# Optimization experiments

Hardware: AMD Instinct MI355X
Metric: run time of the kernel (lower is better)

## Reference

```python
import jax, jax.numpy as jnp
import numpy as np


def setup_inputs() -> dict:
    key = jax.random.key(0)
    ks = jax.random.split(key, 8)
    shapes = [(128, 1, 334, 200), (128, 1, 167, 100), (128, 1, 84, 50),
              (128, 1, 42, 25), (128, 1, 21, 13)]
    # sparsity masks (post-sigmoid / gumbel activations), values in [0,1)
    hs = {f"h{i}": jax.random.uniform(ks[i], s, dtype=jnp.float32)
          for i, s in enumerate(shapes)}
    B, M = 128, 64
    im_dimx, im_dimy = 800, 1333
    # xyxy boxes in image coords: top-left in [0, 0.8*dim), size in [8, 0.2*dim+8)
    x1 = jax.random.uniform(ks[5], (B, M), dtype=jnp.float32) * (0.8 * im_dimx)
    y1 = jax.random.uniform(ks[6], (B, M), dtype=jnp.float32) * (0.8 * im_dimy)
    wh = jax.random.uniform(ks[7], (B, M, 2), dtype=jnp.float32)
    x2 = jnp.minimum(x1 + 8.0 + wh[..., 0] * (0.2 * im_dimx), im_dimx)
    y2 = jnp.minimum(y1 + 8.0 + wh[..., 1] * (0.2 * im_dimy), im_dimy)
    boxes = jnp.stack([x1, y1, x2, y2], axis=-1)  # [B, M, 4]
    inp = dict(hs)
    inp["boxes"] = boxes
    inp["im_dimx"] = im_dimx
    inp["im_dimy"] = im_dimy
    return inp


def _level_loss(hi, boxes, im_dimx, im_dimy):
    # hi: [B, 1, H, W], boxes: [B, M, 4] xyxy in image coords
    B, _, H, W = hi.shape
    scale_x = W / im_dimx
    scale_y = H / im_dimy
    x1 = jnp.clip(jnp.round(boxes[..., 0] * scale_x), 0, W - 1)  # [B, M]
    y1 = jnp.clip(jnp.round(boxes[..., 1] * scale_y), 0, H - 1)
    x2 = jnp.clip(jnp.round(boxes[..., 2] * scale_x), 0, W)
    y2 = jnp.clip(jnp.round(boxes[..., 3] * scale_y), 0, H)
    valid = (x2 > x1) & (y2 > y1)  # degenerate boxes skipped
    ys = jnp.arange(H, dtype=hi.dtype)[None, None, :]
    xs = jnp.arange(W, dtype=hi.dtype)[None, None, :]
    # separable per-box interval indicators; OR over boxes via count > 0
    row = ((ys >= y1[..., None]) & (ys < y2[..., None]) & valid[..., None]).astype(hi.dtype)  # [B,M,H]
    col = ((xs >= x1[..., None]) & (xs < x2[..., None])).astype(hi.dtype)                    # [B,M,W]
    cover = jnp.einsum('bmh,bmw->bhw', row, col)  # overlap count per pixel
    gt = (cover > 0).astype(hi.dtype)             # rectangle fill with 1
    tn_pixel = B * H * W
    pi = jnp.sum(gt) / tn_pixel
    return (jnp.sum(hi) / tn_pixel - pi) ** 2


def reference(h0, h1, h2, h3, h4, boxes, im_dimx, im_dimy):
    hs = (h0, h1, h2, h3, h4)
    losses = [_level_loss(hi, boxes, im_dimx, im_dimy) for hi in hs]
    return sum(losses) / len(losses)
```

## Files before the change

kernel.cpp:

```cpp
#include <hip/hip_runtime.h>

#define NLEV 5
#define BATCH 128
#define NBOX 64

__device__ __constant__ int c_H[NLEV] = {334, 167, 84, 42, 21};
__device__ __constant__ int c_N4[NLEV] = {2137600, 534400, 134400, 33600, 8736};
__device__ __constant__ int c_sb_base[NLEV + 1] = {0, 512, 640, 672, 688, 696};
__device__ __constant__ int c_cb_base[NLEV + 1] = {0, 128, 256, 299, 321, 332};

#define NSUMB 696
#define NCOVB 332
#define NBLOCKS (NSUMB + NCOVB)

#define COV_OFF_BYTES (NSUMB * 8)

__device__ inline unsigned long long maskn(int n) {
  return (n >= 64) ? ~0ull : ((1ull << n) - 1ull);
}
__device__ inline unsigned long long rangemask(int x1, int x2, int base) {
  int lo = min(max(x1 - base, 0), 64);
  int hi = min(max(x2 - base, 0), 64);
  return maskn(hi) & ~maskn(lo);
}

template <int H, int W, int BPB>
__device__ __forceinline__ int cover_compute(
    int lblk, const float* __restrict__ boxes, int dimx, int dimy, int t,
    unsigned long long* __restrict__ s_mask, int2* __restrict__ s_y) {
  constexpr int NW = (W + 63) / 64;
  const float sx = (float)((double)W / (double)dimx);
  const float sy = (float)((double)H / (double)dimy);
  const int b0 = lblk * BPB;

  for (int idx = t; idx < NBOX * BPB; idx += 256) {
    const int m = idx / BPB;
    const int j = idx - m * BPB;
    const int b = b0 + j;
    unsigned long long w[NW];
#pragma unroll
    for (int q = 0; q < NW; ++q) w[q] = 0ull;
    int y1 = 0, y2 = 0;
    if (b < BATCH) {
      const float* bp = boxes + ((size_t)b * NBOX + m) * 4;
      float fx1 = rintf(bp[0] * sx);
      float fy1 = rintf(bp[1] * sy);
      float fx2 = rintf(bp[2] * sx);
      float fy2 = rintf(bp[3] * sy);
      int x1 = (int)fminf(fmaxf(fx1, 0.0f), (float)(W - 1));
      int x2 = (int)fminf(fmaxf(fx2, 0.0f), (float)W);
      y1 = (int)fminf(fmaxf(fy1, 0.0f), (float)(H - 1));
      y2 = (int)fminf(fmaxf(fy2, 0.0f), (float)H);
      if ((x2 > x1) && (y2 > y1)) {
#pragma unroll
        for (int q = 0; q < NW; ++q) w[q] = rangemask(x1, x2, q * 64);
      } else {
        y1 = 0; y2 = 0;
      }
    }
#pragma unroll
    for (int q = 0; q < NW; ++q) s_mask[idx * NW + q] = w[q];
    s_y[idx] = make_int2(y1, y2);
  }
  __syncthreads();

  int local = 0;
  if (BPB == 1) {
    for (int h = t; h < H; h += 256) {
      unsigned long long acc[NW];
#pragma unroll
      for (int q = 0; q < NW; ++q) acc[q] = 0ull;
      for (int m = 0; m < NBOX; ++m) {
        const int2 yr = s_y[m];
        const unsigned long long ym =
            (h >= yr.x && h < yr.y) ? ~0ull : 0ull;
#pragma unroll
        for (int q = 0; q < NW; ++q) acc[q] |= s_mask[m * NW + q] & ym;
      }
#pragma unroll
      for (int q = 0; q < NW; ++q) local += __popcll(acc[q]);
    }
  } else {
    const int j = t / H;
    const int h = t - j * H;
    if (j < BPB && b0 + j < BATCH) {
      unsigned long long acc = 0ull;
      for (int m = 0; m < NBOX; ++m) {
        const int2 yr = s_y[m * BPB + j];
        const unsigned long long ym =
            (h >= yr.x && h < yr.y) ? ~0ull : 0ull;
        acc |= s_mask[m * BPB + j] & ym;
      }
      local = __popcll(acc);
    }
  }
  return local;
}

__global__ __launch_bounds__(256) void fused_kernel(
    const float* __restrict__ h0, const float* __restrict__ h1,
    const float* __restrict__ h2, const float* __restrict__ h3,
    const float* __restrict__ h4, const float* __restrict__ boxes,
    const int* __restrict__ dimx, const int* __restrict__ dimy,
    void* __restrict__ ws) {
  __shared__ unsigned long long s_mask[NBOX * 12];
  __shared__ int2 s_y[NBOX * 12];
  __shared__ double s_red[4];
  __shared__ int s_cnt[4];

  double* __restrict__ sum_part = (double*)ws;
  unsigned int* __restrict__ cov_part =
      (unsigned int*)((char*)ws + COV_OFF_BYTES);
  const int blk = blockIdx.x;
  const int t = threadIdx.x;

  if (blk < NSUMB) {
    int lev = 0;
    while (blk >= c_sb_base[lev + 1]) ++lev;
    const int lblk = blk - c_sb_base[lev];
    const int nblk = c_sb_base[lev + 1] - c_sb_base[lev];
    const float* p;
    switch (lev) {
      case 0: p = h0; break;
      case 1: p = h1; break;
      case 2: p = h2; break;
      case 3: p = h3; break;
      default: p = h4; break;
    }
    const float4* __restrict__ p4 = (const float4*)p;
    const int n4 = c_N4[lev];
    const int stride = nblk * 256;

    double acc = 0.0;
    for (int i = lblk * 256 + t; i < n4; i += stride) {
      float4 v = p4[i];
      acc += (double)v.x;
      acc += (double)v.y;
      acc += (double)v.z;
      acc += (double)v.w;
    }
    for (int off = 32; off > 0; off >>= 1) acc += __shfl_down(acc, off, 64);
    const int wave = t >> 6, lane = t & 63;
    if (lane == 0) s_red[wave] = acc;
    __syncthreads();
    if (t == 0)
      sum_part[blk] = (s_red[0] + s_red[1]) + (s_red[2] + s_red[3]);
  } else {
    const int cb = blk - NSUMB;
    const int dx = dimx[0], dy = dimy[0];
    int local;
    if (cb < c_cb_base[1]) {
      local = cover_compute<334, 200, 1>(cb, boxes, dx, dy, t, s_mask, s_y);
    } else if (cb < c_cb_base[2]) {
      local = cover_compute<167, 100, 1>(cb - 128, boxes, dx, dy, t, s_mask, s_y);
    } else if (cb < c_cb_base[3]) {
      local = cover_compute<84, 50, 3>(cb - 256, boxes, dx, dy, t, s_mask, s_y);
    } else if (cb < c_cb_base[4]) {
      local = cover_compute<42, 25, 6>(cb - 299, boxes, dx, dy, t, s_mask, s_y);
    } else {
      local = cover_compute<21, 13, 12>(cb - 321, boxes, dx, dy, t, s_mask, s_y);
    }
    for (int off = 32; off > 0; off >>= 1) local += __shfl_down(local, off, 64);
    const int wave = t >> 6, lane = t & 63;
    if (lane == 0) s_cnt[wave] = local;
    __syncthreads();
    if (t == 0)
      cov_part[cb] =
          (unsigned int)(s_cnt[0] + s_cnt[1] + s_cnt[2] + s_cnt[3]);
  }
}

__global__ __launch_bounds__(320) void final_kernel(
    const void* __restrict__ ws, float* __restrict__ out) {
  const double* __restrict__ sum_part = (const double*)ws;
  const unsigned int* __restrict__ cov_part =
      (const unsigned int*)((const char*)ws + COV_OFF_BYTES);
  const int wave = threadIdx.x >> 6;
  const int lane = threadIdx.x & 63;
  __shared__ double s_loss[NLEV];
  __device__ __constant__ static const int dummy = 0; (void)dummy;

  const int sb0 = c_sb_base[wave], sb1 = c_sb_base[wave + 1];
  double s = 0.0;
  for (int i = sb0 + lane; i < sb1; i += 64) s += sum_part[i];
  const int cb0 = c_cb_base[wave], cb1 = c_cb_base[wave + 1];
  unsigned int c = 0;
  for (int i = cb0 + lane; i < cb1; i += 64) c += cov_part[i];
  for (int off = 32; off > 0; off >>= 1) {
    s += __shfl_down(s, off, 64);
    c += __shfl_down(c, off, 64);
  }
  if (lane == 0) {
    const int HH[NLEV] = {334, 167, 84, 42, 21};
    const int WW[NLEV] = {200, 100, 50, 25, 13};
    double tn = (double)BATCH * (double)HH[wave] * (double)WW[wave];
    double d = s / tn - (double)c / tn;
    s_loss[wave] = d * d;
  }
  __syncthreads();
  if (threadIdx.x == 0) {
    double acc = 0.0;
    for (int l = 0; l < NLEV; ++l) acc += s_loss[l];
    out[0] = (float)(acc / (double)NLEV);
  }
}

extern "C" void kernel_launch(void* const* d_in, const int* in_sizes, int n_in,
                              void* d_out, int out_size, void* d_ws,
                              size_t ws_size, hipStream_t stream) {
  const float* h0 = (const float*)d_in[0];
  const float* h1 = (const float*)d_in[1];
  const float* h2 = (const float*)d_in[2];
  const float* h3 = (const float*)d_in[3];
  const float* h4 = (const float*)d_in[4];
  const float* boxes = (const float*)d_in[5];
  const int* dimx = (const int*)d_in[6];
  const int* dimy = (const int*)d_in[7];

  fused_kernel<<<NBLOCKS, 256, 0, stream>>>(h0, h1, h2, h3, h4, boxes, dimx,
                                            dimy, d_ws);
  final_kernel<<<1, 320, 0, stream>>>(d_ws, (float*)d_out);
}
```

Baseline: 96.07 us.

## Fuse final reduction into main kernel via cooperative grid sync

Launches the main kernel cooperatively and uses a grid-wide sync so block 0 can perform the final per-level loss reduction, removing the separate second kernel launch. The sum block count is trimmed so the grid can be co-resident (1024 blocks). A fallback keeps the two-kernel path if the cooperative launch fails. The grid sync adds barrier cost and the cooperative launch may carry extra launch overhead.

```diff
diff --git a/kernel.cpp b/kernel.cpp
--- a/kernel.cpp
+++ b/kernel.cpp
@@ -1,15 +1,19 @@
 #include <hip/hip_runtime.h>
+#include <hip/hip_cooperative_groups.h>
+
+namespace cg = cooperative_groups;
 
 #define NLEV 5
 #define BATCH 128
 #define NBOX 64
 
 __device__ __constant__ int c_H[NLEV] = {334, 167, 84, 42, 21};
+__device__ __constant__ int c_W[NLEV] = {200, 100, 50, 25, 13};
 __device__ __constant__ int c_N4[NLEV] = {2137600, 534400, 134400, 33600, 8736};
-__device__ __constant__ int c_sb_base[NLEV + 1] = {0, 512, 640, 672, 688, 696};
+__device__ __constant__ int c_sb_base[NLEV + 1] = {0, 508, 636, 668, 684, 692};
 __device__ __constant__ int c_cb_base[NLEV + 1] = {0, 128, 256, 299, 321, 332};
 
-#define NSUMB 696
+#define NSUMB 692
 #define NCOVB 332
 #define NBLOCKS (NSUMB + NCOVB)
 
@@ -22,6 +26,19 @@
   int lo = min(max(x1 - base, 0), 64);
   int hi = min(max(x2 - base, 0), 64);
   return maskn(hi) & ~maskn(lo);
+}
+
+__device__ inline void store_agent(double* p, double v) {
+  __hip_atomic_store(p, v, __ATOMIC_RELAXED, __HIP_MEMORY_SCOPE_AGENT);
+}
+__device__ inline void store_agent(unsigned int* p, unsigned int v) {
+  __hip_atomic_store(p, v, __ATOMIC_RELAXED, __HIP_MEMORY_SCOPE_AGENT);
+}
+__device__ inline double load_agent(const double* p) {
+  return __hip_atomic_load(p, __ATOMIC_RELAXED, __HIP_MEMORY_SCOPE_AGENT);
+}
+__device__ inline unsigned int load_agent(const unsigned int* p) {
+  return __hip_atomic_load(p, __ATOMIC_RELAXED, __HIP_MEMORY_SCOPE_AGENT);
 }
 
 template <int H, int W, int BPB>
@@ -72,8 +89,7 @@
       for (int q = 0; q < NW; ++q) acc[q] = 0ull;
       for (int m = 0; m < NBOX; ++m) {
         const int2 yr = s_y[m];
-        const unsigned long long ym =
-            (h >= yr.x && h < yr.y) ? ~0ull : 0ull;
+        const unsigned long long ym = (h >= yr.x && h < yr.y) ? ~0ull : 0ull;
 #pragma unroll
         for (int q = 0; q < NW; ++q) acc[q] |= s_mask[m * NW + q] & ym;
       }
@@ -87,8 +103,7 @@
       unsigned long long acc = 0ull;
       for (int m = 0; m < NBOX; ++m) {
         const int2 yr = s_y[m * BPB + j];
-        const unsigned long long ym =
-            (h >= yr.x && h < yr.y) ? ~0ull : 0ull;
+        const unsigned long long ym = (h >= yr.x && h < yr.y) ? ~0ull : 0ull;
         acc |= s_mask[m * BPB + j] & ym;
       }
       local = __popcll(acc);
@@ -97,22 +112,25 @@
   return local;
 }
 
-__global__ __launch_bounds__(256) void fused_kernel(
+template <bool COOP>
+__global__ __launch_bounds__(256) void fused_t(
     const float* __restrict__ h0, const float* __restrict__ h1,
     const float* __restrict__ h2, const float* __restrict__ h3,
     const float* __restrict__ h4, const float* __restrict__ boxes,
     const int* __restrict__ dimx, const int* __restrict__ dimy,
-    void* __restrict__ ws) {
+    void* __restrict__ ws, float* __restrict__ out) {
   __shared__ unsigned long long s_mask[NBOX * 12];
   __shared__ int2 s_y[NBOX * 12];
   __shared__ double s_red[4];
   __shared__ int s_cnt[4];
+  __shared__ double s_loss[NLEV];
 
   double* __restrict__ sum_part = (double*)ws;
   unsigned int* __restrict__ cov_part =
       (unsigned int*)((char*)ws + COV_OFF_BYTES);
   const int blk = blockIdx.x;
   const int t = threadIdx.x;
+  const int wave = t >> 6, lane = t & 63;
 
   if (blk < NSUMB) {
     int lev = 0;
@@ -140,11 +158,11 @@
       acc += (double)v.w;
     }
     for (int off = 32; off > 0; off >>= 1) acc += __shfl_down(acc, off, 64);
-    const int wave = t >> 6, lane = t & 63;
     if (lane == 0) s_red[wave] = acc;
     __syncthreads();
     if (t == 0)
-      sum_part[blk] = (s_red[0] + s_red[1]) + (s_red[2] + s_red[3]);
+      store_agent(&sum_part[blk],
+                  (s_red[0] + s_red[1]) + (s_red[2] + s_red[3]));
   } else {
     const int cb = blk - NSUMB;
     const int dx = dimx[0], dy = dimy[0];
@@ -161,12 +179,41 @@
       local = cover_compute<21, 13, 12>(cb - 321, boxes, dx, dy, t, s_mask, s_y);
     }
     for (int off = 32; off > 0; off >>= 1) local += __shfl_down(local, off, 64);
-    const int wave = t >> 6, lane = t & 63;
     if (lane == 0) s_cnt[wave] = local;
     __syncthreads();
     if (t == 0)
-      cov_part[cb] =
-          (unsigned int)(s_cnt[0] + s_cnt[1] + s_cnt[2] + s_cnt[3]);
+      store_agent(&cov_part[cb],
+                  (unsigned int)(s_cnt[0] + s_cnt[1] + s_cnt[2] + s_cnt[3]));
+  }
+
+  if constexpr (COOP) {
+    __threadfence();
+    cg::this_grid().sync();
+    if (blk == 0) {
+      for (int lev = wave; lev < NLEV; lev += 4) {
+        double s = 0.0;
+        for (int i = c_sb_base[lev] + lane; i < c_sb_base[lev + 1]; i += 64)
+          s += load_agent(&sum_part[i]);
+        unsigned int c = 0;
+        for (int i = c_cb_base[lev] + lane; i < c_cb_base[lev + 1]; i += 64)
+          c += load_agent(&cov_part[i]);
+        for (int off = 32; off > 0; off >>= 1) {
+          s += __shfl_down(s, off, 64);
+          c += __shfl_down(c, off, 64);
+        }
+        if (lane == 0) {
+          double tn = (double)BATCH * (double)c_H[lev] * (double)c_W[lev];
+          double d = s / tn - (double)c / tn;
+          s_loss[lev] = d * d;
+        }
+      }
+      __syncthreads();
+      if (t == 0) {
+        double acc = 0.0;
+        for (int l = 0; l < NLEV; ++l) acc += s_loss[l];
+        out[0] = (float)(acc / (double)NLEV);
+      }
+    }
   }
 }
 
@@ -178,7 +225,6 @@
   const int wave = threadIdx.x >> 6;
   const int lane = threadIdx.x & 63;
   __shared__ double s_loss[NLEV];
-  __device__ __constant__ static const int dummy = 0; (void)dummy;
 
   const int sb0 = c_sb_base[wave], sb1 = c_sb_base[wave + 1];
   double s = 0.0;
@@ -191,9 +237,7 @@
     c += __shfl_down(c, off, 64);
   }
   if (lane == 0) {
-    const int HH[NLEV] = {334, 167, 84, 42, 21};
-    const int WW[NLEV] = {200, 100, 50, 25, 13};
-    double tn = (double)BATCH * (double)HH[wave] * (double)WW[wave];
+    double tn = (double)BATCH * (double)c_H[wave] * (double)c_W[wave];
     double d = s / tn - (double)c / tn;
     s_loss[wave] = d * d;
   }
@@ -216,8 +260,16 @@
   const float* boxes = (const float*)d_in[5];
   const int* dimx = (const int*)d_in[6];
   const int* dimy = (const int*)d_in[7];
-
-  fused_kernel<<<NBLOCKS, 256, 0, stream>>>(h0, h1, h2, h3, h4, boxes, dimx,
-                                            dimy, d_ws);
-  final_kernel<<<1, 320, 0, stream>>>(d_ws, (float*)d_out);
-}
+  void* ws = d_ws;
+  float* out = (float*)d_out;
+
+  void* args[] = {&h0, &h1, &h2, &h3, &h4, &boxes, &dimx, &dimy, &ws, &out};
+  hipError_t err = hipLaunchCooperativeKernel(
+      reinterpret_cast<const void*>(&fused_t<true>), dim3(NBLOCKS), dim3(256),
+      args, 0, stream);
+  if (err != hipSuccess) {
+    fused_t<false><<<NBLOCKS, 256, 0, stream>>>(h0, h1, h2, h3, h4, boxes,
+                                                dimx, dimy, ws, out);
+    final_kernel<<<1, 320, 0, stream>>>(ws, out);
+  }
+}
```

Measured after the change: 325.5 us. 239% more time.
